# Kernel tuning notes

Hardware: AMD Instinct MI355X
Metric: run time of the kernel (lower is better)

Reference implementation:

```python
import jax, jax.numpy as jnp
import numpy as np

B, N, D, H, L, DEG = 8, 4096, 128, 4, 3, 16
C = D // H          # per-head out channels = 32
F = 4 * D           # feedforward hidden = 512
E = B * N * DEG     # 524288 edges, block-diagonal per batch


def setup_inputs() -> dict:
    rng = np.random.default_rng(0)
    # Each flattened node receives DEG incoming edges from random sources in the SAME batch block,
    # mirroring the per-batch nonzero(adj) + offset construction in the torch module.
    tgt = np.repeat(np.arange(B * N, dtype=np.int32), DEG)
    block = (np.arange(B * N, dtype=np.int32) // N).repeat(DEG) * N
    src = rng.integers(0, N, size=E, dtype=np.int32) + block
    edge_index = jnp.asarray(np.stack([src, tgt]), dtype=jnp.int32)

    key = jax.random.key(0)
    ks = jax.random.split(key, 16)
    s = 0.05
    inp = {
        "x": jax.random.normal(ks[0], (B, N, D), jnp.float32),
        "lin_l_w": jax.random.normal(ks[1], (L, D, D), jnp.float32) * s,
        "lin_l_b": jnp.zeros((L, D), jnp.float32),
        "lin_r_w": jax.random.normal(ks[2], (L, D, D), jnp.float32) * s,
        "lin_r_b": jnp.zeros((L, D), jnp.float32),
        "att": jax.random.normal(ks[3], (L, H, C), jnp.float32) * s,
        "gat_bias": jnp.zeros((L, D), jnp.float32),
        "ln1_g": jnp.ones((L, D), jnp.float32),
        "ln1_b": jnp.zeros((L, D), jnp.float32),
        "ff1_w": jax.random.normal(ks[4], (L, D, F), jnp.float32) * s,
        "ff1_b": jnp.zeros((L, F), jnp.float32),
        "ff2_w": jax.random.normal(ks[5], (L, F, D), jnp.float32) * s,
        "ff2_b": jnp.zeros((L, D), jnp.float32),
        "ln2_g": jnp.ones((L, D), jnp.float32),
        "ln2_b": jnp.zeros((L, D), jnp.float32),
        "edge_index": edge_index,
    }
    return inp


def _layer_norm(x, g, b):
    mu = jnp.mean(x, axis=-1, keepdims=True)
    var = jnp.mean((x - mu) ** 2, axis=-1, keepdims=True)
    return (x - mu) * jax.lax.rsqrt(var + 1e-5) * g + b


def _gatv2(xf, src, tgt, Wl, bl, Wr, br, att, bias, nseg):
    # xf: [nseg, D] flattened nodes. GATv2Conv (PyG), add_self_loops=False, concat=True, eval mode.
    gl = (xf @ Wl + bl).reshape(nseg, H, C)   # source transform (x_j)
    gr = (xf @ Wr + br).reshape(nseg, H, C)   # target transform (x_i)
    e = jax.nn.leaky_relu(gl[src] + gr[tgt], negative_slope=0.2)   # [E, H, C]
    logits = jnp.einsum('ehc,hc->eh', e, att)                      # [E, H]
    m = jax.ops.segment_max(logits, tgt, num_segments=nseg)        # softmax over incoming edges
    a = jnp.exp(logits - m[tgt])
    den = jax.ops.segment_sum(a, tgt, num_segments=nseg)
    alpha = a / den[tgt]                                           # [E, H]
    msg = gl[src] * alpha[..., None]                               # [E, H, C]
    out = jax.ops.segment_sum(msg, tgt, num_segments=nseg)         # [nseg, H, C]
    return out.reshape(nseg, H * C) + bias


def reference(x, lin_l_w, lin_l_b, lin_r_w, lin_r_b, att, gat_bias,
              ln1_g, ln1_b, ff1_w, ff1_b, ff2_w, ff2_b, ln2_g, ln2_b,
              edge_index):
    b, n, d = x.shape
    nseg = b * n
    src, tgt = edge_index[0], edge_index[1]
    for l in range(lin_l_w.shape[0]):
        xf = _gatv2(x.reshape(nseg, d), src, tgt,
                    lin_l_w[l], lin_l_b[l], lin_r_w[l], lin_r_b[l],
                    att[l], gat_bias[l], nseg)
        x = xf.reshape(b, n, d)
        h = _layer_norm(x, ln1_g[l], ln1_b[l])
        h = jax.nn.silu(h @ ff1_w[l] + ff1_b[l]) @ ff2_w[l] + ff2_b[l]
        x = _layer_norm(x + h, ln2_g[l], ln2_b[l])
    return x
```

## Files before the change

kernel.cpp:

```cpp
#include <hip/hip_runtime.h>
#include <math.h>

#define BB   8
#define NN   4096
#define DD   128
#define HH   4
#define CC   32
#define LLAY 3
#define DEG  16
#define NSEG (BB*NN)
#define FF   512

typedef __bf16 bf16;
typedef __bf16 bf16x4 __attribute__((ext_vector_type(4)));
typedef __bf16 bf16x8 __attribute__((ext_vector_type(8)));
typedef float  f32x4  __attribute__((ext_vector_type(4)));

template<int ACT, typename OutT>
__global__ __launch_bounds__(256) void mfma_gemm(
    const bf16* __restrict__ A, const bf16* __restrict__ Bt,
    const float* __restrict__ bias, OutT* __restrict__ C,
    int M, int N, int K)
{
    __shared__ bf16 As[128 * 32];
    __shared__ bf16 Bs[128 * 32];

    const int tid  = threadIdx.x;
    const int wave = tid >> 6;
    const int lane = tid & 63;
    const int wr   = wave >> 1;
    const int wc   = wave & 1;
    const int bm   = blockIdx.x * 128;
    const int bn   = blockIdx.y * 128;

    const int lr   = lane & 15;
    const int lkp  = ((lane >> 4) ^ (lane & 3)) * 8;
    const int srow = lane >> 2;
    const int skb  = ((lane & 3) ^ ((lane >> 2) & 3)) * 8;

    f32x4 acc[4][4] = {};

    for (int k0 = 0; k0 < K; k0 += 32) {
        #pragma unroll
        for (int r = 0; r < 2; ++r) {
            int chunk = wave * 2 + r;
            const bf16* ga = A + (size_t)(bm + chunk * 16 + srow) * K + k0 + skb;
            __builtin_amdgcn_global_load_lds(
                (const __attribute__((address_space(1))) void*)ga,
                (__attribute__((address_space(3))) void*)(As + chunk * 512),
                16, 0, 0);
            const bf16* gb = Bt + (size_t)(bn + chunk * 16 + srow) * K + k0 + skb;
            __builtin_amdgcn_global_load_lds(
                (const __attribute__((address_space(1))) void*)gb,
                (__attribute__((address_space(3))) void*)(Bs + chunk * 512),
                16, 0, 0);
        }
        __syncthreads();

        bf16x8 af[4], bfr[4];
        #pragma unroll
        for (int i = 0; i < 4; ++i)
            af[i] = *(const bf16x8*)&As[(wr * 64 + i * 16 + lr) * 32 + lkp];
        #pragma unroll
        for (int j = 0; j < 4; ++j)
            bfr[j] = *(const bf16x8*)&Bs[(wc * 64 + j * 16 + lr) * 32 + lkp];
        #pragma unroll
        for (int i = 0; i < 4; ++i)
            #pragma unroll
            for (int j = 0; j < 4; ++j)
                acc[i][j] = __builtin_amdgcn_mfma_f32_16x16x32_bf16(
                    af[i], bfr[j], acc[i][j], 0, 0, 0);
        __syncthreads();
    }

    const int orow = (lane >> 4) * 4;
    #pragma unroll
    for (int j = 0; j < 4; ++j) {
        int gcol = bn + wc * 64 + j * 16 + lr;
        float bv = bias[gcol];
        #pragma unroll
        for (int i = 0; i < 4; ++i) {
            int grow0 = bm + wr * 64 + i * 16 + orow;
            #pragma unroll
            for (int q = 0; q < 4; ++q) {
                float t = acc[i][j][q] + bv;
                if (ACT == 1) t = t / (1.0f + __expf(-t));
                C[(size_t)(grow0 + q) * N + gcol] = (OutT)t;
            }
        }
    }
}

template<typename OutT>
__global__ __launch_bounds__(256) void ff2_ln_kernel(
    const bf16* __restrict__ A,
    const bf16* __restrict__ Bt,
    const float* __restrict__ bias,
    const float* __restrict__ resid,
    const float* __restrict__ g, const float* __restrict__ b,
    OutT* __restrict__ out)
{
    __shared__ float pool[128 * 128];
    bf16* As = (bf16*)pool;
    bf16* Bs = (bf16*)(pool + 2048);

    const int tid  = threadIdx.x;
    const int wave = tid >> 6;
    const int lane = tid & 63;
    const int wr   = wave >> 1;
    const int wc   = wave & 1;
    const int bm   = blockIdx.x * 128;

    const int lr   = lane & 15;
    const int lkp  = ((lane >> 4) ^ (lane & 3)) * 8;
    const int srow = lane >> 2;
    const int skb  = ((lane & 3) ^ ((lane >> 2) & 3)) * 8;

    f32x4 acc[4][4] = {};

    for (int k0 = 0; k0 < 512; k0 += 32) {
        #pragma unroll
        for (int r = 0; r < 2; ++r) {
            int chunk = wave * 2 + r;
            const bf16* ga = A + (size_t)(bm + chunk * 16 + srow) * 512 + k0 + skb;
            __builtin_amdgcn_global_load_lds(
                (const __attribute__((address_space(1))) void*)ga,
                (__attribute__((address_space(3))) void*)(As + chunk * 512),
                16, 0, 0);
            const bf16* gb = Bt + (size_t)(chunk * 16 + srow) * 512 + k0 + skb;
            __builtin_amdgcn_global_load_lds(
                (const __attribute__((address_space(1))) void*)gb,
                (__attribute__((address_space(3))) void*)(Bs + chunk * 512),
                16, 0, 0);
        }
        __syncthreads();

        bf16x8 af[4], bfr[4];
        #pragma unroll
        for (int i = 0; i < 4; ++i)
            af[i] = *(const bf16x8*)&As[(wr * 64 + i * 16 + lr) * 32 + lkp];
        #pragma unroll
        for (int j = 0; j < 4; ++j)
            bfr[j] = *(const bf16x8*)&Bs[(wc * 64 + j * 16 + lr) * 32 + lkp];
        #pragma unroll
        for (int i = 0; i < 4; ++i)
            #pragma unroll
            for (int j = 0; j < 4; ++j)
                acc[i][j] = __builtin_amdgcn_mfma_f32_16x16x32_bf16(
                    af[i], bfr[j], acc[i][j], 0, 0, 0);
        __syncthreads();
    }

    const int orow = (lane >> 4) * 4;
    #pragma unroll
    for (int j = 0; j < 4; ++j) {
        int col = wc * 64 + j * 16 + lr;
        float bv = bias[col];
        #pragma unroll
        for (int i = 0; i < 4; ++i) {
            int row0 = wr * 64 + i * 16 + orow;
            #pragma unroll
            for (int q = 0; q < 4; ++q)
                pool[(row0 + q) * 128 + col] = acc[i][j][q] + bv;
        }
    }
    __syncthreads();

    const int c0 = lane * 2;
    for (int it = 0; it < 32; ++it) {
        int row = wave * 32 + it;
        float2 v = { pool[row * 128 + c0], pool[row * 128 + c0 + 1] };
        float2 r = *(const float2*)(resid + (size_t)(bm + row) * DD + c0);
        v.x += r.x; v.y += r.y;

        float s = v.x + v.y;
        #pragma unroll
        for (int mk = 1; mk < 64; mk <<= 1) s += __shfl_xor(s, mk);
        const float mu = s * (1.0f / 128.0f);
        float dx = v.x - mu, dy = v.y - mu;
        float q = dx * dx + dy * dy;
        #pragma unroll
        for (int mk = 1; mk < 64; mk <<= 1) q += __shfl_xor(q, mk);
        const float rs = rsqrtf(q * (1.0f / 128.0f) + 1e-5f);

        out[(size_t)(bm + row) * DD + c0]     = (OutT)(dx * rs * g[c0]     + b[c0]);
        out[(size_t)(bm + row) * DD + c0 + 1] = (OutT)(dy * rs * g[c0 + 1] + b[c0 + 1]);
    }
}

#define CVT_XN  1048576
__global__ __launch_bounds__(256) void cvt_all(
    const float* __restrict__ x,
    const float* __restrict__ ll_w, const float* __restrict__ ll_b,
    const float* __restrict__ lr_w, const float* __restrict__ lr_b,
    const float* __restrict__ ff1_w, const float* __restrict__ ff2_w,
    bf16* __restrict__ xb, bf16* __restrict__ wlr,
    bf16* __restrict__ wt1, bf16* __restrict__ wt2, float* __restrict__ blr)
{
    int gid = blockIdx.x * 256 + threadIdx.x;
    if (gid < CVT_XN) {
        int i = gid * 4;
        float4 v = *(const float4*)(x + i);
        bf16x4 o = { (bf16)v.x, (bf16)v.y, (bf16)v.z, (bf16)v.w };
        *(bf16x4*)(xb + i) = o;
        return;
    }
    int idx = gid - CVT_XN;
    if (idx < 98304) {
        int l = idx / 32768, e = idx % 32768;
        int n = e >> 7, k = e & 127;
        float v = (n < 128) ? ll_w[l * 16384 + k * 128 + n]
                            : lr_w[l * 16384 + k * 128 + (n - 128)];
        wlr[idx] = (bf16)v;
    } else if (idx < 294912) {
        int r = idx - 98304;
        int l = r >> 16, e = r & 65535;
        int k = e >> 9, n = e & 511;
        wt1[l * 65536 + n * 128 + k] = (bf16)ff1_w[l * 65536 + k * 512 + n];
    } else if (idx < 491520) {
        int r = idx - 294912;
        int l = r >> 16, e = r & 65535;
        int k = e >> 7, n = e & 127;
        wt2[l * 65536 + n * 512 + k] = (bf16)ff2_w[l * 65536 + k * 128 + n];
    } else if (idx < 492288) {
        int r = idx - 491520;
        int l = r / 256, n = r % 256;
        blr[r] = (n < 128) ? ll_b[l * 128 + n] : lr_b[l * 128 + (n - 128)];
    }
}

__global__ __launch_bounds__(256) void gat_ln_kernel(
    const float* __restrict__ glr,
    const int* __restrict__ src, const float* __restrict__ att,
    const float* __restrict__ bias,
    const float* __restrict__ ln_g, const float* __restrict__ ln_b,
    float* __restrict__ xg, bf16* __restrict__ ln_out)
{
    const int wave = threadIdx.x >> 6;
    const int lane = threadIdx.x & 63;
    const int bid  = blockIdx.x;
    const int sb   = ((bid & 7) << 10) | (bid >> 3);
    const int node = sb * 4 + wave;
    const int c0   = lane * 2;
    const int h    = lane >> 4;

    const float2 gri = *(const float2*)(glr + (size_t)node * 256 + 128 + c0);
    const float a0 = att[h * CC + (c0 & 31)];
    const float a1 = att[h * CC + ((c0 + 1) & 31)];

    int sidx[DEG];
    const int* sp = src + node * DEG;
    #pragma unroll
    for (int e = 0; e < DEG; ++e) sidx[e] = sp[e];

    float glx[DEG], gly[DEG], logit[DEG];

    #pragma unroll
    for (int e = 0; e < DEG; ++e) {
        float2 gv = *(const float2*)(glr + (size_t)sidx[e] * 256 + c0);
        glx[e] = gv.x; gly[e] = gv.y;
        float s0 = gv.x + gri.x, s1 = gv.y + gri.y;
        float v0 = fmaxf(s0, 0.2f * s0);
        float v1 = fmaxf(s1, 0.2f * s1);
        float p = v0 * a0 + v1 * a1;
        p += __shfl_xor(p, 1);
        p += __shfl_xor(p, 2);
        p += __shfl_xor(p, 4);
        p += __shfl_xor(p, 8);
        logit[e] = p;
    }

    float m = logit[0];
    #pragma unroll
    for (int e = 1; e < DEG; ++e) m = fmaxf(m, logit[e]);

    float den = 0.0f, accx = 0.0f, accy = 0.0f;
    #pragma unroll
    for (int e = 0; e < DEG; ++e) {
        float a = __expf(logit[e] - m);
        den += a;
        accx = fmaf(a, glx[e], accx);
        accy = fmaf(a, gly[e], accy);
    }
    float inv = 1.0f / den;
    float2 o;
    o.x = accx * inv + bias[c0];
    o.y = accy * inv + bias[c0 + 1];
    *(float2*)(xg + (size_t)node * DD + c0) = o;

    float s = o.x + o.y;
    #pragma unroll
    for (int mk = 1; mk < 64; mk <<= 1) s += __shfl_xor(s, mk);
    const float mu = s * (1.0f / 128.0f);
    float dx = o.x - mu, dy = o.y - mu;
    float q = dx * dx + dy * dy;
    #pragma unroll
    for (int mk = 1; mk < 64; mk <<= 1) q += __shfl_xor(q, mk);
    const float rs = rsqrtf(q * (1.0f / 128.0f) + 1e-5f);

    ln_out[(size_t)node * DD + c0]     = (bf16)(dx * rs * ln_g[c0]     + ln_b[c0]);
    ln_out[(size_t)node * DD + c0 + 1] = (bf16)(dy * rs * ln_g[c0 + 1] + ln_b[c0 + 1]);
}

extern "C" void kernel_launch(void* const* d_in, const int* in_sizes, int n_in,
                              void* d_out, int out_size, void* d_ws, size_t ws_size,
                              hipStream_t stream)
{
    const float* x        = (const float*)d_in[0];
    const float* lin_l_w  = (const float*)d_in[1];
    const float* lin_l_b  = (const float*)d_in[2];
    const float* lin_r_w  = (const float*)d_in[3];
    const float* lin_r_b  = (const float*)d_in[4];
    const float* att      = (const float*)d_in[5];
    const float* gat_bias = (const float*)d_in[6];
    const float* ln1_g    = (const float*)d_in[7];
    const float* ln1_b    = (const float*)d_in[8];
    const float* ff1_w    = (const float*)d_in[9];
    const float* ff1_b    = (const float*)d_in[10];
    const float* ff2_w    = (const float*)d_in[11];
    const float* ff2_b    = (const float*)d_in[12];
    const float* ln2_g    = (const float*)d_in[13];
    const float* ln2_b    = (const float*)d_in[14];
    const int*   src      = (const int*)d_in[15];

    float* out = (float*)d_out;
    float* ws  = (float*)d_ws;

    const size_t NV = (size_t)NSEG * DD;
    float* GLR  = ws;
    float* XG   = GLR + 2 * NV;
    bf16*  XB   = (bf16*)(XG + NV);
    bf16*  LN1B = XB + NV;
    bf16*  HID  = LN1B + NV;
    bf16*  WLR  = HID + (size_t)NSEG * FF;
    bf16*  WT1  = WLR + (size_t)LLAY * 256 * DD;
    bf16*  WT2  = WT1 + (size_t)LLAY * FF * DD;
    float* BLR  = (float*)(WT2 + (size_t)LLAY * DD * FF);

    cvt_all<<<6018, 256, 0, stream>>>(x, lin_l_w, lin_l_b, lin_r_w, lin_r_b,
                                      ff1_w, ff2_w, XB, WLR, WT1, WT2, BLR);

    for (int l = 0; l < LLAY; ++l) {
        dim3 gLin(NSEG / 128, 256 / 128);
        mfma_gemm<0, float><<<gLin, 256, 0, stream>>>(XB, WLR + (size_t)l*256*DD,
                                                      BLR + l*256, GLR, NSEG, 256, DD);
        gat_ln_kernel<<<NSEG / 4, 256, 0, stream>>>(GLR, src, att + l*HH*CC,
                                                    gat_bias + l*DD,
                                                    ln1_g + l*DD, ln1_b + l*DD,
                                                    XG, LN1B);
        dim3 gF1(NSEG / 128, FF / 128);
        mfma_gemm<1, bf16><<<gF1, 256, 0, stream>>>(LN1B, WT1 + (size_t)l*FF*DD,
                                                    ff1_b + l*FF, HID, NSEG, FF, DD);
        if (l == LLAY - 1) {
            ff2_ln_kernel<float><<<NSEG / 128, 256, 0, stream>>>(
                HID, WT2 + (size_t)l*DD*FF, ff2_b + l*DD, XG,
                ln2_g + l*DD, ln2_b + l*DD, out);
        } else {
            ff2_ln_kernel<bf16><<<NSEG / 128, 256, 0, stream>>>(
                HID, WT2 + (size_t)l*DD*FF, ff2_b + l*DD, XG,
                ln2_g + l*DD, ln2_b + l*DD, XB);
        }
    }
}
```

Baseline: 393.6 us.

## Compute GAT attention logits with one lane per edge-head instead of shuffle reductions

Attention logits are now computed with each lane owning one (edge, head) pair, reading 32 channels via float4 loads and reducing serially. Softmax max and sum then use only 4-step shuffles across the 16 edges. The alpha values are broadcast by shuffle, and source features are gathered a second time for the weighted sum. This removes the 64 shuffle-add reductions per node, at the cost of a second gather of the source rows, which will mostly hit in cache.

Measured after the change: 509.6 us. 29.5% more time.

```diff
diff --git a/kernel.cpp b/kernel.cpp
--- a/kernel.cpp
+++ b/kernel.cpp
@@ -241,51 +241,57 @@
     const int bid  = blockIdx.x;
     const int sb   = ((bid & 7) << 10) | (bid >> 3);
     const int node = sb * 4 + wave;
-    const int c0   = lane * 2;
+    const int e    = lane & 15;
     const int h    = lane >> 4;
 
-    const float2 gri = *(const float2*)(glr + (size_t)node * 256 + 128 + c0);
-    const float a0 = att[h * CC + (c0 & 31)];
-    const float a1 = att[h * CC + ((c0 + 1) & 31)];
-
-    int sidx[DEG];
+    const int   se  = src[node * DEG + e];
+    const float* glp = glr + (size_t)se   * 256 + h * CC;
+    const float* grp = glr + (size_t)node * 256 + 128 + h * CC;
+    const float* ap  = att + h * CC;
+
+    float lg = 0.0f;
+    #pragma unroll
+    for (int c4 = 0; c4 < 8; ++c4) {
+        float4 gv = *(const float4*)(glp + c4 * 4);
+        float4 rv = *(const float4*)(grp + c4 * 4);
+        float4 av = *(const float4*)(ap  + c4 * 4);
+        float t;
+        t = gv.x + rv.x; t = fmaxf(t, 0.2f * t); lg = fmaf(t, av.x, lg);
+        t = gv.y + rv.y; t = fmaxf(t, 0.2f * t); lg = fmaf(t, av.y, lg);
+        t = gv.z + rv.z; t = fmaxf(t, 0.2f * t); lg = fmaf(t, av.z, lg);
+        t = gv.w + rv.w; t = fmaxf(t, 0.2f * t); lg = fmaf(t, av.w, lg);
+    }
+
+    float m = lg;
+    m = fmaxf(m, __shfl_xor(m, 1));
+    m = fmaxf(m, __shfl_xor(m, 2));
+    m = fmaxf(m, __shfl_xor(m, 4));
+    m = fmaxf(m, __shfl_xor(m, 8));
+    float p = __expf(lg - m);
+    float den = p;
+    den += __shfl_xor(den, 1);
+    den += __shfl_xor(den, 2);
+    den += __shfl_xor(den, 4);
+    den += __shfl_xor(den, 8);
+    const float alpha = p / den;
+
+    const int c0 = lane * 2;
+    float al[DEG];
+    #pragma unroll
+    for (int k = 0; k < DEG; ++k)
+        al[k] = __shfl(alpha, (lane & 48) | k);
+
     const int* sp = src + node * DEG;
-    #pragma unroll
-    for (int e = 0; e < DEG; ++e) sidx[e] = sp[e];
-
-    float glx[DEG], gly[DEG], logit[DEG];
-
-    #pragma unroll
-    for (int e = 0; e < DEG; ++e) {
-        float2 gv = *(const float2*)(glr + (size_t)sidx[e] * 256 + c0);
-        glx[e] = gv.x; gly[e] = gv.y;
-        float s0 = gv.x + gri.x, s1 = gv.y + gri.y;
-        float v0 = fmaxf(s0, 0.2f * s0);
-        float v1 = fmaxf(s1, 0.2f * s1);
-        float p = v0 * a0 + v1 * a1;
-        p += __shfl_xor(p, 1);
-        p += __shfl_xor(p, 2);
-        p += __shfl_xor(p, 4);
-        p += __shfl_xor(p, 8);
-        logit[e] = p;
-    }
-
-    float m = logit[0];
-    #pragma unroll
-    for (int e = 1; e < DEG; ++e) m = fmaxf(m, logit[e]);
-
-    float den = 0.0f, accx = 0.0f, accy = 0.0f;
-    #pragma unroll
-    for (int e = 0; e < DEG; ++e) {
-        float a = __expf(logit[e] - m);
-        den += a;
-        accx = fmaf(a, glx[e], accx);
-        accy = fmaf(a, gly[e], accy);
-    }
-    float inv = 1.0f / den;
+    float accx = 0.0f, accy = 0.0f;
+    #pragma unroll
+    for (int k = 0; k < DEG; ++k) {
+        float2 gv = *(const float2*)(glr + (size_t)sp[k] * 256 + c0);
+        accx = fmaf(al[k], gv.x, accx);
+        accy = fmaf(al[k], gv.y, accy);
+    }
     float2 o;
-    o.x = accx * inv + bias[c0];
-    o.y = accy * inv + bias[c0 + 1];
+    o.x = accx + bias[c0];
+    o.y = accy + bias[c0 + 1];
     *(float2*)(xg + (size_t)node * DD + c0) = o;
 
     float s = o.x + o.y;
```
